# Optimization experiments

Measured on AMD Instinct MI355X. Metric: run time of the kernel, lower is better.

Reference implementation:

```python
import jax, jax.numpy as jnp
import numpy as np

DIM = 1024
HEADS = 16
HEAD_DIM = DIM // HEADS
K_NEIGH = 64  # local_window, adaptive_window=False
SCALE = 1.0 / np.sqrt(HEAD_DIM)


def setup_inputs() -> dict:
    key = jax.random.key(0)
    ks = jax.random.split(key, 6)
    b, n = 1, 4096
    x = jax.random.normal(ks[0], (b, n, DIM), dtype=jnp.float32)
    cantor_coords = jax.random.uniform(ks[1], (n,), dtype=jnp.float32)
    # torch nn.Linear(dim, 3*dim): weight [3*dim, dim]; we store transposed [dim, 3*dim]
    W_qkv = jax.random.normal(ks[2], (DIM, 3 * DIM), dtype=jnp.float32) * (1.0 / np.sqrt(DIM))
    b_qkv = jax.random.normal(ks[3], (3 * DIM,), dtype=jnp.float32) * 0.01
    W_out = jax.random.normal(ks[4], (DIM, DIM), dtype=jnp.float32) * (1.0 / np.sqrt(DIM))
    b_out = jax.random.normal(ks[5], (DIM,), dtype=jnp.float32) * 0.01
    return {"x": x, "cantor_coords": cantor_coords, "W_qkv": W_qkv,
            "b_qkv": b_qkv, "W_out": W_out, "b_out": b_out}


def _routes(cantor_coords):
    # [n, n] pairwise |c_i - c_j|; k smallest -> top_k of negated distances
    d = jnp.abs(cantor_coords[:, None] - cantor_coords[None, :])
    _, idx = jax.lax.top_k(-d, K_NEIGH)  # [n, k]
    return idx


def reference(x, cantor_coords, W_qkv, b_qkv, W_out, b_out):
    b, n, _ = x.shape
    qkv = x @ W_qkv + b_qkv                          # [b, n, 3*dim]
    qkv = qkv.reshape(b, n, 3, HEADS, HEAD_DIM)
    qkv = jnp.transpose(qkv, (2, 0, 3, 1, 4))        # [3, b, h, n, d]
    q, k, v = qkv[0], qkv[1], qkv[2]

    routes = _routes(cantor_coords)                  # [n, k]
    k_g = k[:, :, routes, :]                         # [b, h, n, k, d]
    v_g = v[:, :, routes, :]
    scores = jnp.einsum('bhqd,bhqkd->bhqk', q, k_g) * SCALE
    attn = jax.nn.softmax(scores, axis=-1)           # dropout p=0 (eval)
    out = jnp.einsum('bhqk,bhqkd->bhqd', attn, v_g)  # [b, h, n, d]
    out = jnp.transpose(out, (0, 2, 1, 3)).reshape(b, n, DIM)
    return out @ W_out + b_out
```

## Files before the change

### kernel.cpp

```cpp
#include <hip/hip_runtime.h>
#include <hip/hip_bf16.h>

typedef _Float16 f16x8 __attribute__((ext_vector_type(8)));
typedef float f32x4 __attribute__((ext_vector_type(4)));
typedef unsigned long long u64;

#define NSEQ 4096
#define DIMM 1024
#define NHEAD 16
#define HD 64
#define NQKV 3072

#define BAR() asm volatile("s_barrier" ::: "memory")

__device__ __forceinline__ f32x4 mfma16(f16x8 a, f16x8 b, f32x4 c) {
  return __builtin_amdgcn_mfma_f32_16x16x32_f16(a, b, c, 0, 0, 0);
}

__device__ __forceinline__ void glds16(const void* g, void* l) {
  __builtin_amdgcn_global_load_lds(
      (const __attribute__((address_space(1))) void*)g,
      (__attribute__((address_space(3))) void*)l, 16, 0, 0);
}

__global__ __launch_bounds__(256) void prep_kernel(
    const float* __restrict__ x, _Float16* __restrict__ xh,
    const float* __restrict__ Wqkv, _Float16* __restrict__ wqkvt,
    const float* __restrict__ Wout, _Float16* __restrict__ woutt,
    const float* __restrict__ cc, int* __restrict__ sorted_idx,
    float* __restrict__ csort) {
  __shared__ __align__(16) char plds[16640];
  const int bid = blockIdx.x, t = threadIdx.x;
  if (bid < 2048) {
    const int i = bid * 256 + t;
    const float4 a = ((const float4*)x)[i * 2];
    const float4 b = ((const float4*)x)[i * 2 + 1];
    f16x8 o = {(_Float16)a.x, (_Float16)a.y, (_Float16)a.z, (_Float16)a.w,
               (_Float16)b.x, (_Float16)b.y, (_Float16)b.z, (_Float16)b.w};
    ((f16x8*)xh)[i] = o;
  } else if (bid < 3072) {
    const bool qkv = bid < 2816;
    const int sub = qkv ? bid - 2048 : bid - 2816;
    const float* W = qkv ? Wqkv : Wout;
    _Float16* Wt = qkv ? wqkvt : woutt;
    const int Nn = qkv ? 3072 : 1024;
    const int k0 = (sub & 15) * 64, n0 = (sub >> 4) * 64;
    float (*tile)[65] = (float(*)[65])plds;
    const int tx = t & 63, ty = t >> 6;
    for (int rr = ty; rr < 64; rr += 4)
      tile[rr][tx] = W[(size_t)(k0 + rr) * Nn + n0 + tx];
    __syncthreads();
    for (int ccn = ty; ccn < 64; ccn += 4)
      Wt[(size_t)(n0 + ccn) * 1024 + k0 + tx] = (_Float16)tile[tx][ccn];
  } else {
    float* sc = (float*)plds;
#pragma unroll
    for (int it = 0; it < 4; ++it) {
      const int i = it * 256 + t;
      ((float4*)sc)[i] = ((const float4*)cc)[i];
    }
    __syncthreads();
    const int elem = (bid - 3072) * 32 + (t >> 3);
    const int s = t & 7;
    const unsigned mybits = __float_as_uint(sc[elem]);
    int cnt = 0;
#pragma unroll 8
    for (int m = 0; m < 512; ++m) {
      const int j = s + (m << 3);
      const unsigned bj = __float_as_uint(sc[j]);
      cnt += (bj < mybits || (bj == mybits && j < elem)) ? 1 : 0;
    }
    cnt += __shfl_xor(cnt, 1);
    cnt += __shfl_xor(cnt, 2);
    cnt += __shfl_xor(cnt, 4);
    if (s == 0) {
      sorted_idx[cnt] = elem;
      csort[cnt] = sc[elem];
    }
  }
}

__global__ __launch_bounds__(256) void mask_kernel(
    const float* __restrict__ csort, const int* __restrict__ sorted_idx,
    unsigned* __restrict__ masks) {
  __shared__ unsigned lm[4][8];
  const int tid = threadIdx.x, lane = tid & 63, wid = tid >> 6;
  const int p = blockIdx.x * 4 + wid;
  int W0 = 64 * (p >> 6) - 96;
  W0 = min(max(W0, 0), NSEQ - 256);
  const float cp = csort[p];
  u64 key[4];
#pragma unroll
  for (int r = 0; r < 4; ++r) {
    const int w = r * 64 + lane;
    const float d = fabsf(csort[W0 + w] - cp);
    key[r] = (((u64)__float_as_uint(d)) << 20) |
             (((u64)(unsigned)sorted_idx[W0 + w]) << 8) | (unsigned)w;
  }
  if (lane < 8) lm[wid][lane] = 0u;
#pragma unroll
  for (int k = 2; k <= 256; k <<= 1) {
#pragma unroll
    for (int j = k >> 1; j > 0; j >>= 1) {
      if (j >= 64) {
        const int rj = j >> 6;
#pragma unroll
        for (int r = 0; r < 4; ++r) {
          const int rp = r ^ rj;
          if (rp > r) {
            const bool up = (((r * 64) & k) == 0);
            const u64 a = key[r], b2 = key[rp];
            const bool sw = (a > b2) == up;
            key[r] = sw ? b2 : a;
            key[rp] = sw ? a : b2;
          }
        }
      } else {
#pragma unroll
        for (int r = 0; r < 4; ++r) {
          const u64 pv = __shfl_xor(key[r], j);
          const bool up = (((r * 64 + lane) & k) == 0);
          const bool lower = ((lane & j) == 0);
          const bool takemin = (lower == up);
          const u64 mn = key[r] < pv ? key[r] : pv;
          const u64 mx = key[r] < pv ? pv : key[r];
          key[r] = takemin ? mn : mx;
        }
      }
    }
  }
  const unsigned w0 = (unsigned)(key[0] & 0xffu);
  atomicOr(&lm[wid][w0 >> 5], 1u << (w0 & 31u));
  __syncthreads();
  if (lane < 8) masks[p * 8 + lane] = lm[wid][lane];
}

__device__ __forceinline__ f16x8 ldsfrag(const char* base, int r, int g) {
  return *(const f16x8*)(base + r * 128 + ((g ^ (r & 7)) << 4));
}

__device__ __forceinline__ void stage_half(const char* gbase, size_t kb, int t,
                                           char* lds_half, int tid) {
#pragma unroll
  for (int s = 0; s < 2; ++s) {
    const int rel = tid * 16 + s * 8192;
    const int r = rel >> 7;
    const int g = (rel >> 4) & 7;
    const int gg = g ^ (r & 7);
    glds16(gbase + (size_t)r * kb + t * 128 + gg * 16, lds_half + rel);
  }
}

__device__ __forceinline__ void stage_64r(const char* gbase, size_t kb, int t,
                                          char* lds8k, int tid) {
  const int rel = tid * 16;
  const int r = rel >> 7;
  const int g = (rel >> 4) & 7;
  const int gg = g ^ (r & 7);
  glds16(gbase + (size_t)r * kb + t * 128 + gg * 16, lds8k + rel);
}

__device__ __forceinline__ void rd_b3(const char* Bb, int wn, int lr, int kg,
                                      f16x8 (&bf)[3][2]) {
#pragma unroll
  for (int nt = 0; nt < 3; ++nt) {
    bf[nt][0] = ldsfrag(Bb, wn + nt * 16 + lr, kg);
    bf[nt][1] = ldsfrag(Bb, wn + nt * 16 + lr, 4 + kg);
  }
}

template <int Q>
__device__ __forceinline__ void rd_a(const char* Ab, int wm, int lr, int kg,
                                     f16x8 (&af)[2][2]) {
#pragma unroll
  for (int m = 0; m < 2; ++m) {
    af[m][0] = ldsfrag(Ab, wm + (2 * Q + m) * 16 + lr, kg);
    af[m][1] = ldsfrag(Ab, wm + (2 * Q + m) * 16 + lr, 4 + kg);
  }
}

template <int Q>
__device__ __forceinline__ void do_mfma3(const f16x8 (&af)[2][2],
                                         const f16x8 (&bf)[3][2],
                                         f32x4 (&acc)[8][3]) {
#pragma unroll
  for (int m = 0; m < 2; ++m)
#pragma unroll
    for (int nt = 0; nt < 3; ++nt) {
      acc[2 * Q + m][nt] = mfma16(af[m][0], bf[nt][0], acc[2 * Q + m][nt]);
      acc[2 * Q + m][nt] = mfma16(af[m][1], bf[nt][1], acc[2 * Q + m][nt]);
    }
}

template <bool LAST>
__device__ __forceinline__ void ktile_pair192(const char* Ag, const char* Bg,
                                              size_t kb, char* smem, int tid,
                                              int wm, int wn, int lr, int kg,
                                              int t1, int t2, int t3,
                                              f32x4 (&acc)[8][3]) {
  char* A0 = smem;
  char* A1 = smem + 32768;
  char* B0 = smem + 65536;
  char* B1 = smem + 65536 + 24576;
  f16x8 bf[3][2], af[2][2];
  rd_b3(B0, wn, lr, kg, bf);
  rd_a<0>(A0, wm, lr, kg, af);
  stage_64r(Ag, kb, t1, A1, tid);
  stage_64r(Ag + 64 * kb, kb, t1, A1 + 8192, tid);
  BAR();
  __builtin_amdgcn_s_setprio(1);
  do_mfma3<0>(af, bf, acc);
  __builtin_amdgcn_s_setprio(0);
  BAR();
  rd_a<1>(A0, wm, lr, kg, af);
  stage_64r(Ag + 128 * kb, kb, t1, A1 + 16384, tid);
  stage_64r(Ag + 192 * kb, kb, t1, A1 + 24576, tid);
  BAR();
  __builtin_amdgcn_s_setprio(1);
  do_mfma3<1>(af, bf, acc);
  __builtin_amdgcn_s_setprio(0);
  BAR();
  rd_a<2>(A0, wm, lr, kg, af);
  if (!LAST) {
    stage_64r(Bg, kb, t2, B0, tid);
    stage_64r(Bg + 64 * kb, kb, t2, B0 + 8192, tid);
  }
  BAR();
  __builtin_amdgcn_s_setprio(1);
  do_mfma3<2>(af, bf, acc);
  __builtin_amdgcn_s_setprio(0);
  BAR();
  rd_a<3>(A0, wm, lr, kg, af);
  if (!LAST) stage_64r(Bg + 128 * kb, kb, t2, B0 + 16384, tid);
  BAR();
  __builtin_amdgcn_s_setprio(1);
  do_mfma3<3>(af, bf, acc);
  __builtin_amdgcn_s_setprio(0);
  if (LAST)
    asm volatile("s_waitcnt vmcnt(0)" ::: "memory");
  else
    asm volatile("s_waitcnt vmcnt(3)" ::: "memory");
  BAR();
  rd_b3(B1, wn, lr, kg, bf);
  rd_a<0>(A1, wm, lr, kg, af);
  if (!LAST) {
    stage_64r(Ag, kb, t2, A0, tid);
    stage_64r(Ag + 64 * kb, kb, t2, A0 + 8192, tid);
  }
  BAR();
  __builtin_amdgcn_s_setprio(1);
  do_mfma3<0>(af, bf, acc);
  __builtin_amdgcn_s_setprio(0);
  BAR();
  rd_a<1>(A1, wm, lr, kg, af);
  if (!LAST) {
    stage_64r(Ag + 128 * kb, kb, t2, A0 + 16384, tid);
    stage_64r(Ag + 192 * kb, kb, t2, A0 + 24576, tid);
  }
  BAR();
  __builtin_amdgcn_s_setprio(1);
  do_mfma3<1>(af, bf, acc);
  __builtin_amdgcn_s_setprio(0);
  BAR();
  rd_a<2>(A1, wm, lr, kg, af);
  if (!LAST) {
    stage_64r(Bg, kb, t3, B1, tid);
    stage_64r(Bg + 64 * kb, kb, t3, B1 + 8192, tid);
  }
  BAR();
  __builtin_amdgcn_s_setprio(1);
  do_mfma3<2>(af, bf, acc);
  __builtin_amdgcn_s_setprio(0);
  BAR();
  rd_a<3>(A1, wm, lr, kg, af);
  if (!LAST) stage_64r(Bg + 128 * kb, kb, t3, B1 + 16384, tid);
  BAR();
  __builtin_amdgcn_s_setprio(1);
  do_mfma3<3>(af, bf, acc);
  __builtin_amdgcn_s_setprio(0);
  if (!LAST) asm volatile("s_waitcnt vmcnt(3)" ::: "memory");
  BAR();
}

__global__ __launch_bounds__(512, 2) void qkv_gemm192_kernel(
    const _Float16* __restrict__ A, const _Float16* __restrict__ Bt,
    const float* __restrict__ bias, _Float16* __restrict__ C) {
  extern __shared__ char smem[];
  const int NN = 3072;
  const size_t kb = 2048;
  const int tid = threadIdx.x;
  const int lane = tid & 63, wid = tid >> 6;
  const int lr = lane & 15, kg = lane >> 4;
  const int wm = (wid >> 2) * 128, wn = (wid & 3) * 48;
  const int bid = blockIdx.x;
  const int flat = (bid & 7) * 32 + (bid >> 3);
  const int bx = flat >> 4, by = flat & 15;
  const int m0 = bx * 256, n0 = by * 192;
  const char* Ag = (const char*)A + (size_t)m0 * kb;
  const char* Bg = (const char*)Bt + (size_t)n0 * kb;
  char* A0 = smem;
  char* B0 = smem + 65536;
  char* B1 = smem + 65536 + 24576;
  f32x4 acc[8][3] = {};
#pragma unroll
  for (int u = 0; u < 4; ++u)
    stage_64r(Ag + (size_t)(64 * u) * kb, kb, 0, A0 + u * 8192, tid);
#pragma unroll
  for (int u = 0; u < 3; ++u)
    stage_64r(Bg + (size_t)(64 * u) * kb, kb, 0, B0 + u * 8192, tid);
#pragma unroll
  for (int u = 0; u < 3; ++u)
    stage_64r(Bg + (size_t)(64 * u) * kb, kb, 1, B1 + u * 8192, tid);
  asm volatile("s_waitcnt vmcnt(3)" ::: "memory");
  BAR();
#pragma unroll 1
  for (int i = 0; i < 7; ++i)
    ktile_pair192<false>(Ag, Bg, kb, smem, tid, wm, wn, lr, kg, 2 * i + 1,
                         2 * i + 2, 2 * i + 3, acc);
  ktile_pair192<true>(Ag, Bg, kb, smem, tid, wm, wn, lr, kg, 15, 16, 17, acc);
#pragma unroll
  for (int nt = 0; nt < 3; ++nt) {
    const int col = n0 + wn + nt * 16 + lr;
    const float bv = bias[col];
#pragma unroll
    for (int mt = 0; mt < 8; ++mt) {
      const int row0 = m0 + wm + mt * 16 + kg * 4;
#pragma unroll
      for (int rr = 0; rr < 4; ++rr)
        C[(size_t)(row0 + rr) * NN + col] = (_Float16)(acc[mt][nt][rr] + bv);
    }
  }
}

__global__ __launch_bounds__(512, 2) void out_gemm128_kernel(
    const _Float16* __restrict__ A, const _Float16* __restrict__ Bt,
    const float* __restrict__ bias, float* __restrict__ C) {
  extern __shared__ char smem[];
  const size_t kb = 2048;
  const int tid = threadIdx.x;
  const int lane = tid & 63, wid = tid >> 6;
  const int lr = lane & 15, kg = lane >> 4;
  const int wm = (wid >> 2) * 64, wn = (wid & 3) * 32;
  const int bid = blockIdx.x;
  const int flat = (bid & 7) * 32 + (bid >> 3);
  const int bx = flat >> 3, by = flat & 7;
  const int m0 = bx * 128, n0 = by * 128;
  const char* Ag = (const char*)A + (size_t)m0 * kb;
  const char* Bg = (const char*)Bt + (size_t)n0 * kb;
  f32x4 acc[4][2] = {};
  stage_half(Ag, kb, 0, smem, tid);
  stage_half(Bg, kb, 0, smem + 49152, tid);
  stage_half(Ag, kb, 1, smem + 16384, tid);
  stage_half(Bg, kb, 1, smem + 49152 + 16384, tid);
  asm volatile("s_waitcnt vmcnt(4)" ::: "memory");
  BAR();
#pragma unroll
  for (int t = 0; t < 16; ++t) {
    const char* At = smem + (t % 3) * 16384;
    const char* Bb = smem + 49152 + (t % 3) * 16384;
    f16x8 bf[2][2], af[4][2];
#pragma unroll
    for (int nt = 0; nt < 2; ++nt) {
      bf[nt][0] = ldsfrag(Bb, wn + nt * 16 + lr, kg);
      bf[nt][1] = ldsfrag(Bb, wn + nt * 16 + lr, 4 + kg);
    }
#pragma unroll
    for (int m = 0; m < 4; ++m) {
      af[m][0] = ldsfrag(At, wm + m * 16 + lr, kg);
      af[m][1] = ldsfrag(At, wm + m * 16 + lr, 4 + kg);
    }
    if (t < 14) {
      stage_half(Ag, kb, t + 2, smem + ((t + 2) % 3) * 16384, tid);
      stage_half(Bg, kb, t + 2, smem + 49152 + ((t + 2) % 3) * 16384, tid);
    }
    BAR();
    __builtin_amdgcn_s_setprio(1);
#pragma unroll
    for (int m = 0; m < 4; ++m)
#pragma unroll
      for (int nt = 0; nt < 2; ++nt) {
        acc[m][nt] = mfma16(af[m][0], bf[nt][0], acc[m][nt]);
        acc[m][nt] = mfma16(af[m][1], bf[nt][1], acc[m][nt]);
      }
    __builtin_amdgcn_s_setprio(0);
    if (t < 14)
      asm volatile("s_waitcnt vmcnt(4)" ::: "memory");
    else if (t == 14)
      asm volatile("s_waitcnt vmcnt(0)" ::: "memory");
    BAR();
  }
#pragma unroll
  for (int nt = 0; nt < 2; ++nt) {
    const int col = n0 + wn + nt * 16 + lr;
    const float bv = bias[col];
#pragma unroll
    for (int mt = 0; mt < 4; ++mt) {
      const int row0 = m0 + wm + mt * 16 + kg * 4;
#pragma unroll
      for (int rr = 0; rr < 4; ++rr)
        C[(size_t)(row0 + rr) * 1024 + col] = acc[mt][nt][rr] + bv;
    }
  }
}

__global__ __launch_bounds__(256) void permute_v_kernel(
    const _Float16* __restrict__ qkvh, const int* __restrict__ sorted_idx,
    _Float16* __restrict__ Vts) {
  __shared__ _Float16 vt[64][66];
  const int h = blockIdx.x & 15;
  const int P0 = (blockIdx.x >> 4) * 64;
  const int tid = threadIdx.x;
#pragma unroll
  for (int it = 0; it < 2; ++it) {
    const int i = it * 256 + tid;
    const int row = i >> 3, seg = i & 7;
    const int orig = sorted_idx[P0 + row];
    f16x8 v8 = *(const f16x8*)(qkvh + (size_t)orig * NQKV + 2048 + h * 64 + seg * 8);
#pragma unroll
    for (int e = 0; e < 8; ++e) vt[row][seg * 8 + e] = v8[e];
  }
  __syncthreads();
#pragma unroll
  for (int it = 0; it < 2; ++it) {
    const int i = it * 256 + tid;
    const int d = i >> 3, seg = i & 7;
    f16x8 o;
#pragma unroll
    for (int e = 0; e < 8; ++e) o[e] = vt[seg * 8 + e][d];
    *(f16x8*)(Vts + ((size_t)h * 64 + d) * NSEQ + P0 + seg * 8) = o;
  }
}

__global__ __launch_bounds__(256) void attn_kernel(
    const _Float16* __restrict__ qkvh, const _Float16* __restrict__ Vts,
    const unsigned* __restrict__ masks, const int* __restrict__ sorted_idx,
    _Float16* __restrict__ attn_h) {
  __shared__ __align__(128) char sK[32768];
  __shared__ __align__(128) char sV[32768];
  const int flat = (blockIdx.x & 7) * 128 + (blockIdx.x >> 3);
  const int b = flat & 63, h = flat >> 6;
  const int tid = threadIdx.x, lane = tid & 63, wid = tid >> 6;
  const int W0 = min(max(64 * b - 96, 0), NSEQ - 256);
  const int lrow16 = lane & 15, kgrp = lane >> 4;
  int ridx[8];
#pragma unroll
  for (int c = 0; c < 8; ++c)
    ridx[c] = sorted_idx[W0 + c * 32 + wid * 8 + (lane >> 3)];
#pragma unroll
  for (int c = 0; c < 8; ++c) {
    const int o = c * 4096 + wid * 1024 + lane * 16;
    const int row = o >> 7;
    const int inrow = (o & 127) ^ ((row & 7) << 4);
    glds16((const char*)qkvh + (size_t)ridx[c] * 6144 + 2048 + h * 128 + inrow,
           sK + o);
    const int d = o >> 9;
    const int inrowv = (o & 511) ^ ((d & 7) << 4);
    glds16((const char*)Vts + (size_t)(h * 64 + d) * (NSEQ * 2) + W0 * 2 + inrowv,
           sV + o);
  }
  const int p_base = b * 64 + wid * 16;
  const int orig_q = sorted_idx[p_base + lrow16];
  const char* qp = (const char*)qkvh + (size_t)orig_q * 6144 + h * 128 + kgrp * 16;
  const f16x8 aq0 = *(const f16x8*)qp;
  const f16x8 aq1 = *(const f16x8*)(qp + 64);
  unsigned mb[4];
#pragma unroll
  for (int r = 0; r < 4; ++r) {
    const int p = p_base + kgrp * 4 + r;
    unsigned bits = 0;
#pragma unroll
    for (int n = 0; n < 16; ++n) {
      const int widx = n * 16 + lrow16;
      bits |= ((masks[p * 8 + (widx >> 5)] >> (widx & 31)) & 1u) << n;
    }
    mb[r] = bits;
  }
  __syncthreads();
  float sv[16][4];
#pragma unroll
  for (int n = 0; n < 16; ++n) {
    const int j = n * 16 + lrow16;
    const int sw = (j & 7) << 4;
    const char* kr = sK + j * 128;
    const f16x8 b0 = *(const f16x8*)(kr + ((kgrp * 16) ^ sw));
    const f16x8 b1 = *(const f16x8*)(kr + ((64 + kgrp * 16) ^ sw));
    f32x4 a = {};
    a = mfma16(aq0, b0, a);
    a = mfma16(aq1, b1, a);
#pragma unroll
    for (int r = 0; r < 4; ++r)
      sv[n][r] = ((mb[r] >> n) & 1u) ? a[r] * 0.125f : -1e30f;
  }
#pragma unroll
  for (int r = 0; r < 4; ++r) {
    float m = sv[0][r];
#pragma unroll
    for (int n = 1; n < 16; ++n) m = fmaxf(m, sv[n][r]);
    m = fmaxf(m, __shfl_xor(m, 1));
    m = fmaxf(m, __shfl_xor(m, 2));
    m = fmaxf(m, __shfl_xor(m, 4));
    m = fmaxf(m, __shfl_xor(m, 8));
    float s = 0.f;
#pragma unroll
    for (int n = 0; n < 16; ++n) {
      const float e = __expf(sv[n][r] - m);
      sv[n][r] = e;
      s += e;
    }
    s += __shfl_xor(s, 1);
    s += __shfl_xor(s, 2);
    s += __shfl_xor(s, 4);
    s += __shfl_xor(s, 8);
    const float rinv = 1.f / s;
#pragma unroll
    for (int n = 0; n < 16; ++n) sv[n][r] *= rinv;
  }
  __syncthreads();
#pragma unroll
  for (int n = 0; n < 16; ++n) {
#pragma unroll
    for (int r = 0; r < 4; ++r) {
      const int lr = wid * 16 + kgrp * 4 + r;
      const int cb = (n * 16 + lrow16) * 2;
      *(_Float16*)(sK + lr * 512 + (cb ^ ((lr & 7) << 4))) = (_Float16)sv[n][r];
    }
  }
  __syncthreads();
  f32x4 oacc[4] = {};
  const int arow = wid * 16 + lrow16;
  const int swa = (arow & 7) << 4;
#pragma unroll
  for (int kt = 0; kt < 8; ++kt) {
    const int kbo = kt * 64 + kgrp * 16;
    const f16x8 pa = *(const f16x8*)(sK + arow * 512 + (kbo ^ swa));
#pragma unroll
    for (int nt = 0; nt < 4; ++nt) {
      const int d = nt * 16 + lrow16;
      const f16x8 vb = *(const f16x8*)(sV + d * 512 + (kbo ^ ((d & 7) << 4)));
      oacc[nt] = mfma16(pa, vb, oacc[nt]);
    }
  }
#pragma unroll
  for (int r = 0; r < 4; ++r) {
    const int p = p_base + kgrp * 4 + r;
    const int orig = sorted_idx[p];
    _Float16* op = attn_h + (size_t)orig * DIMM + h * 64;
#pragma unroll
    for (int nt = 0; nt < 4; ++nt)
      op[nt * 16 + lrow16] = (_Float16)oacc[nt][r];
  }
}

extern "C" void kernel_launch(void* const* d_in, const int* in_sizes, int n_in,
                              void* d_out, int out_size, void* d_ws, size_t ws_size,
                              hipStream_t stream) {
  const float* x = (const float*)d_in[0];
  const float* cc = (const float*)d_in[1];
  const float* Wqkv = (const float*)d_in[2];
  const float* bqkv = (const float*)d_in[3];
  const float* Wout = (const float*)d_in[4];
  const float* bout = (const float*)d_in[5];
  char* ws = (char*)d_ws;

  _Float16* xh = (_Float16*)(ws + 0);
  _Float16* wqkvt = (_Float16*)(ws + 8388608);
  _Float16* woutt = (_Float16*)(ws + 14680064);
  _Float16* qkvh = (_Float16*)(ws + 16777216);
  _Float16* Vtsb = (_Float16*)(ws + 41943040);
  _Float16* atnh = (_Float16*)(ws + 50331648);
  int* sidx = (int*)(ws + 58720256);
  float* csort = (float*)(ws + 58736640);
  unsigned* msk = (unsigned*)(ws + 58753024);

  hipFuncSetAttribute((const void*)qkv_gemm192_kernel,
                      hipFuncAttributeMaxDynamicSharedMemorySize, 114688);
  hipFuncSetAttribute((const void*)out_gemm128_kernel,
                      hipFuncAttributeMaxDynamicSharedMemorySize, 98304);

  prep_kernel<<<3200, 256, 0, stream>>>(x, xh, Wqkv, wqkvt, Wout, woutt, cc,
                                        sidx, csort);
  mask_kernel<<<1024, 256, 0, stream>>>(csort, sidx, msk);
  qkv_gemm192_kernel<<<256, 512, 114688, stream>>>(xh, wqkvt, bqkv, qkvh);
  permute_v_kernel<<<1024, 256, 0, stream>>>(qkvh, sidx, Vtsb);
  attn_kernel<<<1024, 256, 0, stream>>>(qkvh, Vtsb, msk, sidx, atnh);
  out_gemm128_kernel<<<256, 512, 98304, stream>>>(atnh, woutt, bout,
                                                  (float*)d_out);
}
```

Baseline: 109.8 us.

## Fuse V permute/transpose into attention kernel and vectorize mask loads

Removes the separate permute_v kernel that gathered V rows by sorted index and wrote a transposed copy to global memory. The attention kernel now gathers V rows directly into registers and scatters them transposed into swizzled LDS with scalar 16-bit stores. Mask words are also loaded as two uint4 vectors instead of per-bit scalar loads. This saves one launch and a global round trip, at the cost of slower element-wise LDS transposition stores and extra register pressure.

```diff
diff --git a/kernel.cpp b/kernel.cpp
--- a/kernel.cpp
+++ b/kernel.cpp
@@ -403,38 +403,9 @@
   }
 }
 
-__global__ __launch_bounds__(256) void permute_v_kernel(
-    const _Float16* __restrict__ qkvh, const int* __restrict__ sorted_idx,
-    _Float16* __restrict__ Vts) {
-  __shared__ _Float16 vt[64][66];
-  const int h = blockIdx.x & 15;
-  const int P0 = (blockIdx.x >> 4) * 64;
-  const int tid = threadIdx.x;
-#pragma unroll
-  for (int it = 0; it < 2; ++it) {
-    const int i = it * 256 + tid;
-    const int row = i >> 3, seg = i & 7;
-    const int orig = sorted_idx[P0 + row];
-    f16x8 v8 = *(const f16x8*)(qkvh + (size_t)orig * NQKV + 2048 + h * 64 + seg * 8);
-#pragma unroll
-    for (int e = 0; e < 8; ++e) vt[row][seg * 8 + e] = v8[e];
-  }
-  __syncthreads();
-#pragma unroll
-  for (int it = 0; it < 2; ++it) {
-    const int i = it * 256 + tid;
-    const int d = i >> 3, seg = i & 7;
-    f16x8 o;
-#pragma unroll
-    for (int e = 0; e < 8; ++e) o[e] = vt[seg * 8 + e][d];
-    *(f16x8*)(Vts + ((size_t)h * 64 + d) * NSEQ + P0 + seg * 8) = o;
-  }
-}
-
 __global__ __launch_bounds__(256) void attn_kernel(
-    const _Float16* __restrict__ qkvh, const _Float16* __restrict__ Vts,
-    const unsigned* __restrict__ masks, const int* __restrict__ sorted_idx,
-    _Float16* __restrict__ attn_h) {
+    const _Float16* __restrict__ qkvh, const unsigned* __restrict__ masks,
+    const int* __restrict__ sorted_idx, _Float16* __restrict__ attn_h) {
   __shared__ __align__(128) char sK[32768];
   __shared__ __align__(128) char sV[32768];
   const int flat = (blockIdx.x & 7) * 128 + (blockIdx.x >> 3);
@@ -453,10 +424,13 @@
     const int inrow = (o & 127) ^ ((row & 7) << 4);
     glds16((const char*)qkvh + (size_t)ridx[c] * 6144 + 2048 + h * 128 + inrow,
            sK + o);
-    const int d = o >> 9;
-    const int inrowv = (o & 511) ^ ((d & 7) << 4);
-    glds16((const char*)Vts + (size_t)(h * 64 + d) * (NSEQ * 2) + W0 * 2 + inrowv,
-           sV + o);
+  }
+  f16x8 vreg[8];
+#pragma unroll
+  for (int c = 0; c < 8; ++c) {
+    const int o = c * 4096 + wid * 1024 + lane * 16;
+    vreg[c] = *(const f16x8*)((const char*)qkvh + (size_t)ridx[c] * 6144 +
+                              4096 + h * 128 + (o & 127));
   }
   const int p_base = b * 64 + wid * 16;
   const int orig_q = sorted_idx[p_base + lrow16];
@@ -467,13 +441,25 @@
 #pragma unroll
   for (int r = 0; r < 4; ++r) {
     const int p = p_base + kgrp * 4 + r;
+    const uint4 wa = *(const uint4*)&masks[p * 8];
+    const uint4 wb = *(const uint4*)&masks[p * 8 + 4];
+    const unsigned wsv[8] = {wa.x, wa.y, wa.z, wa.w, wb.x, wb.y, wb.z, wb.w};
     unsigned bits = 0;
 #pragma unroll
-    for (int n = 0; n < 16; ++n) {
-      const int widx = n * 16 + lrow16;
-      bits |= ((masks[p * 8 + (widx >> 5)] >> (widx & 31)) & 1u) << n;
-    }
+    for (int n = 0; n < 16; ++n)
+      bits |= ((wsv[n >> 1] >> (((n & 1) << 4) + lrow16)) & 1u) << n;
     mb[r] = bits;
+  }
+#pragma unroll
+  for (int c = 0; c < 8; ++c) {
+    const int o = c * 4096 + wid * 1024 + lane * 16;
+    const int k = o >> 7;
+    const int d0 = (o & 127) >> 1;
+#pragma unroll
+    for (int e = 0; e < 8; ++e) {
+      const int d = d0 + e;
+      *(_Float16*)(sV + d * 512 + ((2 * k) ^ ((d & 7) << 4))) = vreg[c][e];
+    }
   }
   __syncthreads();
   float sv[16][4];
@@ -566,11 +552,10 @@
   _Float16* wqkvt = (_Float16*)(ws + 8388608);
   _Float16* woutt = (_Float16*)(ws + 14680064);
   _Float16* qkvh = (_Float16*)(ws + 16777216);
-  _Float16* Vtsb = (_Float16*)(ws + 41943040);
-  _Float16* atnh = (_Float16*)(ws + 50331648);
-  int* sidx = (int*)(ws + 58720256);
-  float* csort = (float*)(ws + 58736640);
-  unsigned* msk = (unsigned*)(ws + 58753024);
+  _Float16* atnh = (_Float16*)(ws + 41943040);
+  int* sidx = (int*)(ws + 50331648);
+  float* csort = (float*)(ws + 50348032);
+  unsigned* msk = (unsigned*)(ws + 50364416);
 
   hipFuncSetAttribute((const void*)qkv_gemm192_kernel,
                       hipFuncAttributeMaxDynamicSharedMemorySize, 114688);
@@ -581,8 +566,7 @@
                                         sidx, csort);
   mask_kernel<<<1024, 256, 0, stream>>>(csort, sidx, msk);
   qkv_gemm192_kernel<<<256, 512, 114688, stream>>>(xh, wqkvt, bqkv, qkvh);
-  permute_v_kernel<<<1024, 256, 0, stream>>>(qkvh, sidx, Vtsb);
-  attn_kernel<<<1024, 256, 0, stream>>>(qkvh, Vtsb, msk, sidx, atnh);
+  attn_kernel<<<1024, 256, 0, stream>>>(qkvh, msk, sidx, atnh);
   out_gemm128_kernel<<<256, 512, 98304, stream>>>(atnh, woutt, bout,
                                                   (float*)d_out);
 }
```

New measurement: 109.6 us. No clear change (-0.1%).
